# Optimization experiments

Measured on AMD Instinct MI355X. Metric: run time of the kernel, lower is better.

## Reference

```python
import jax, jax.numpy as jnp
import numpy as np

T, B, E, H = 2048, 4, 1024, 16
HD = E // H
SCALE = HD ** -0.5


def setup_inputs() -> dict:
    key = jax.random.key(0)
    k1, k2, k3 = jax.random.split(key, 3)
    # xavier-ish scaling on weights for numerical sanity
    inputs = jax.random.normal(k1, (T, B, E), dtype=jnp.float32)
    in_proj_weight = jax.random.normal(k2, (3 * E, E), dtype=jnp.float32) * (2.0 / (4 * E)) ** 0.5
    out_proj_weight = jax.random.normal(k3, (E, E), dtype=jnp.float32) * (1.0 / E) ** 0.5
    return {"inputs": inputs, "in_proj_weight": in_proj_weight, "out_proj_weight": out_proj_weight}


def reference(inputs, in_proj_weight, out_proj_weight):
    t, b, e = inputs.shape
    # fused QKV projection: [T,B,E] @ [E,3E] -> [T, B*H, 3, HD]
    qkv = jnp.einsum('tbe,fe->tbf', inputs, in_proj_weight)
    qkv = qkv.reshape(t, b * H, 3, HD)
    q, k, v = qkv[:, :, 0, :], qkv[:, :, 1, :], qkv[:, :, 2, :]  # [T, B*H, HD]
    # scaled attention scores per (batch*head): [B*H, T, T]
    scores = SCALE * jnp.einsum('tnd,snd->nts', q, k)
    probs = jax.nn.softmax(scores, axis=-1)
    # dropout p=0.0 -> identity
    ctx = jnp.einsum('nts,snd->tnd', probs, v).reshape(t, b, e)
    # output projection (applied to attention context, matching intended math / backward)
    return jnp.einsum('tbe,oe->tbo', ctx, out_proj_weight)
```

## Files before the change

kernel.cpp:

```cpp
#include <hip/hip_runtime.h>
#include <stdint.h>
#include <stddef.h>


typedef __attribute__((ext_vector_type(8))) short bf16x8;
typedef __attribute__((ext_vector_type(4))) float f32x4;
typedef __attribute__((ext_vector_type(4))) unsigned int u32x4;

#define MFMA16(a, b, c) __builtin_amdgcn_mfma_f32_16x16x32_bf16((a), (b), (c), 0, 0, 0)

__device__ __forceinline__ unsigned short f2bf(float f) {
  unsigned u = __builtin_bit_cast(unsigned, f);
  u += 0x7fffu + ((u >> 16) & 1u);
  return (unsigned short)(u >> 16);
}

__device__ __forceinline__ float fast_exp2(float x) {
#if __has_builtin(__builtin_amdgcn_exp2f)
  return __builtin_amdgcn_exp2f(x);
#else
  return exp2f(x);
#endif
}

__device__ __forceinline__ unsigned cvtpk(float lo, float hi) {
  unsigned r;
  asm volatile("v_cvt_pk_bf16_f32 %0, %1, %2" : "=v"(r) : "v"(lo), "v"(hi));
  return r;
}

__device__ __forceinline__ void lane_swap32(unsigned &a, unsigned &b) {
#if __has_builtin(__builtin_amdgcn_permlane32_swap)
  auto r = __builtin_amdgcn_permlane32_swap(a, b, false, false);
  a = r[0]; b = r[1];
#else
  const bool hi = (threadIdx.x & 32) != 0;
  unsigned sa = (unsigned)__shfl_xor((int)a, 32, 64);
  unsigned sb = (unsigned)__shfl_xor((int)b, 32, 64);
  unsigned na = hi ? sb : a;
  unsigned nb = hi ? b : sa;
  a = na; b = nb;
#endif
}

__device__ __forceinline__ void lane_swap16(unsigned &a, unsigned &b) {
#if __has_builtin(__builtin_amdgcn_permlane16_swap)
  auto r = __builtin_amdgcn_permlane16_swap(a, b, false, false);
  a = r[0]; b = r[1];
#else
  const bool odd = (threadIdx.x & 16) != 0;
  unsigned sa = (unsigned)__shfl_xor((int)a, 16, 64);
  unsigned sb = (unsigned)__shfl_xor((int)b, 16, 64);
  unsigned na = odd ? sb : a;
  unsigned nb = odd ? b : sa;
  a = na; b = nb;
#endif
}

__device__ __forceinline__ void gload_lds16(const void* g, void* l) {
  __builtin_amdgcn_global_load_lds((const __attribute__((address_space(1))) void*)g,
                                   (__attribute__((address_space(3))) void*)l,
                                   16, 0, 0);
}

__global__ __launch_bounds__(256) void k_cvt(const float* __restrict__ src,
                                             unsigned short* __restrict__ dst, int n4) {
  int i = blockIdx.x * 256 + threadIdx.x;
  if (i >= n4) return;
  const float4 v = ((const float4*)src)[i];
  ushort4 o;
  o.x = f2bf(v.x); o.y = f2bf(v.y); o.z = f2bf(v.z); o.w = f2bf(v.w);
  ((ushort4*)dst)[i] = o;
}

__global__ __launch_bounds__(256, 2) void k_gemm_qkv(
    const unsigned short* __restrict__ A,
    const unsigned short* __restrict__ Bt,
    unsigned short* __restrict__ Qb,
    unsigned short* __restrict__ Kb,
    unsigned short* __restrict__ Vb) {
  constexpr int K = 1024;
  __shared__ __align__(16) unsigned short As[128 * 32];
  __shared__ __align__(16) unsigned short Bs[128 * 32];
  const int tid = threadIdx.x;
  const int l = tid & 63, w = tid >> 6;
  const int lr = l & 15, lg = l >> 4;
  const int bm = blockIdx.x, bn = blockIdx.y;
  const int wr = (w >> 1) * 64, wc = (w & 1) * 64;

  f32x4 acc[4][4] = {};

  const int o0 = tid * 16, o1 = tid * 16 + 4096;
  const int r0 = o0 >> 6, c0 = o0 & 63;
  const int r1 = o1 >> 6, c1 = o1 & 63;
  const char* gA0 = (const char*)A + (size_t)(bm * 128 + r0) * (K * 2) + c0;
  const char* gA1 = (const char*)A + (size_t)(bm * 128 + r1) * (K * 2) + c1;
  const char* gB0 = (const char*)Bt + (size_t)(bn * 128 + r0) * (K * 2) + c0;
  const char* gB1 = (const char*)Bt + (size_t)(bn * 128 + r1) * (K * 2) + c1;
  char* lA0 = (char*)As + o0;
  char* lA1 = (char*)As + o1;
  char* lB0 = (char*)Bs + o0;
  char* lB1 = (char*)Bs + o1;

  for (int kt = 0; kt < K / 32; ++kt) {
    const int kb = kt * 64;
    gload_lds16(gA0 + kb, lA0);
    gload_lds16(gA1 + kb, lA1);
    gload_lds16(gB0 + kb, lB0);
    gload_lds16(gB1 + kb, lB1);
    __syncthreads();
    bf16x8 af[4], bfr[4];
#pragma unroll
    for (int mf = 0; mf < 4; ++mf)
      af[mf] = *(const bf16x8*)&As[(wr + mf * 16 + lr) * 32 + lg * 8];
#pragma unroll
    for (int nf = 0; nf < 4; ++nf)
      bfr[nf] = *(const bf16x8*)&Bs[(wc + nf * 16 + lr) * 32 + lg * 8];
#pragma unroll
    for (int mf = 0; mf < 4; ++mf)
#pragma unroll
      for (int nf = 0; nf < 4; ++nf)
        acc[mf][nf] = MFMA16(af[mf], bfr[nf], acc[mf][nf]);
    __syncthreads();
  }

#pragma unroll
  for (int nf = 0; nf < 4; ++nf) {
    const int f = bn * 128 + wc + nf * 16 + lr;
    const int hq = f / 192;
    const int s3 = (f >> 6) % 3;
    const int d = f & 63;
    unsigned short* dst = (s3 == 0) ? Qb : (s3 == 1) ? Kb : Vb;
    const float qscale = (s3 == 0) ? 0.18033688011112042f : 1.0f;
#pragma unroll
    for (int mf = 0; mf < 4; ++mf) {
#pragma unroll
      for (int i = 0; i < 4; ++i) {
        const int r = bm * 128 + wr + mf * 16 + lg * 4 + i;
        const int t = r >> 2, bb2 = r & 3;
        const int nIdx = bb2 * 16 + hq;
        dst[((size_t)nIdx * 2048 + t) * 64 + d] = f2bf(acc[mf][nf][i] * qscale);
      }
    }
  }
}

__global__ __launch_bounds__(256) void k_vtrans(const unsigned short* __restrict__ V,
                                                unsigned short* __restrict__ VT) {
  __shared__ unsigned short tile[64][66];
  const int tid = threadIdx.x;
  const int n = blockIdx.y, t0 = blockIdx.x * 64;
  const int r = tid >> 2, c0 = (tid & 3) * 16;
  const unsigned short* src = V + ((size_t)(n * 2048 + t0 + r) * 64 + c0);
  bf16x8 a = *(const bf16x8*)src;
  bf16x8 b = *(const bf16x8*)(src + 8);
#pragma unroll
  for (int j = 0; j < 8; ++j) tile[r][c0 + j] = (unsigned short)a[j];
#pragma unroll
  for (int j = 0; j < 8; ++j) tile[r][c0 + 8 + j] = (unsigned short)b[j];
  __syncthreads();
  const int d = tid >> 2, u0 = (tid & 3) * 16;
  bf16x8 oA, oB;
#pragma unroll
  for (int j = 0; j < 8; ++j) oA[j] = (short)tile[u0 + j][d];
#pragma unroll
  for (int j = 0; j < 8; ++j) oB[j] = (short)tile[u0 + 8 + j][d];
  unsigned short* dst = VT + ((size_t)(n * 64 + d) * 2048 + t0 + u0);
  *(bf16x8*)dst = oA;
  *(bf16x8*)(dst + 8) = oB;
}

__global__ __launch_bounds__(256, 2) void k_attn(
    const unsigned short* __restrict__ Qb, const unsigned short* __restrict__ Kb,
    const unsigned short* __restrict__ VTb, unsigned short* __restrict__ Cx) {
  __shared__ __align__(16) unsigned short Ks[2][64 * 64];
  __shared__ __align__(16) unsigned short Vt[2][64 * 64];

  const int tid = threadIdx.x;
  const int l = tid & 63, w = tid >> 6;
  const int lq = l & 15, lg = l >> 4;
  const int n = blockIdx.x, qt = blockIdx.y;

  const unsigned short* Qh = Qb + (size_t)n * (2048 * 64);
  const unsigned short* Kh = Kb + (size_t)n * (2048 * 64);
  const unsigned short* Vh = VTb + (size_t)n * (64 * 2048);

  bf16x8 aq[4][2];
#pragma unroll
  for (int qf = 0; qf < 4; ++qf)
#pragma unroll
    for (int kd = 0; kd < 2; ++kd)
      aq[qf][kd] = *(const bf16x8*)&Qh[(size_t)(qt * 256 + w * 64 + qf * 16 + lq) * 64 +
                                       kd * 32 + lg * 8];

  f32x4 o[4][4] = {};
  float lsum[4] = {0.f, 0.f, 0.f, 0.f};

  char* Ksl = (char*)&Ks[0][0];
  char* Vtl = (char*)&Vt[0][0];

  auto STAGE = [&](int buf, int st) {
    const int s0 = st * 64;
#pragma unroll
    for (int it = 0; it < 2; ++it) {
      const int off = (it * 256 + tid) * 16;
      const int row = off >> 7;
      const int colb = (off & 127) ^ ((row & 7) << 4);
      gload_lds16((const char*)Kh + ((size_t)(s0 + row) << 7) + colb, Ksl + buf * 8192 + off);
      gload_lds16((const char*)Vh + ((size_t)row << 12) + (s0 << 1) + colb, Vtl + buf * 8192 + off);
    }
  };

  STAGE(0, 0);
  asm volatile("s_waitcnt vmcnt(0)" ::: "memory");
  __builtin_amdgcn_s_barrier();

#pragma unroll 2
  for (int st = 0; st < 32; ++st) {
    const int cur = st & 1;
    if (st + 1 < 32) STAGE(cur ^ 1, st + 1);

    const char* Kc = Ksl + cur * 8192;
    const char* Vc = Vtl + cur * 8192;

    __builtin_amdgcn_s_setprio(1);
#pragma unroll
    for (int kb = 0; kb < 2; ++kb) {
      bf16x8 kf[2][2];
#pragma unroll
      for (int sfl = 0; sfl < 2; ++sfl) {
        const int rowk = (2 * kb + sfl) * 16 + lq;
        const int sw = (rowk & 7) << 4;
        kf[sfl][0] = *(const bf16x8*)(Kc + ((rowk * 128 + lg * 16) ^ sw));
        kf[sfl][1] = *(const bf16x8*)(Kc + ((rowk * 128 + 64 + lg * 16) ^ sw));
      }

      bf16x8 pq[4];
#pragma unroll
      for (int qf = 0; qf < 4; ++qf) {
        f32x4 s0 = {0.f, 0.f, 0.f, 0.f};
        f32x4 s1 = {0.f, 0.f, 0.f, 0.f};
        s0 = MFMA16(kf[0][0], aq[qf][0], s0);
        s0 = MFMA16(kf[0][1], aq[qf][1], s0);
        s1 = MFMA16(kf[1][0], aq[qf][0], s1);
        s1 = MFMA16(kf[1][1], aq[qf][1], s1);
        float accs = 0.f;
#pragma unroll
        for (int i = 0; i < 4; ++i) {
          s0[i] = fast_exp2(s0[i]);
          s1[i] = fast_exp2(s1[i]);
          accs += s0[i] + s1[i];
        }
        lsum[qf] += accs;
        unsigned w0 = cvtpk(s0[0], s0[1]);
        unsigned w1 = cvtpk(s0[2], s0[3]);
        unsigned w2 = cvtpk(s1[0], s1[1]);
        unsigned w3 = cvtpk(s1[2], s1[3]);
        lane_swap32(w0, w2);
        lane_swap32(w1, w3);
        lane_swap16(w0, w2);
        lane_swap16(w1, w3);
        u32x4 t4 = {w0, w1, w2, w3};
        pq[qf] = __builtin_bit_cast(bf16x8, t4);
      }

#pragma unroll
      for (int df = 0; df < 4; ++df) {
        const int rowd = df * 16 + lq;
        const int sw = (rowd & 7) << 4;
        bf16x8 vf = *(const bf16x8*)(Vc + ((rowd * 128 + kb * 64 + lg * 16) ^ sw));
#pragma unroll
        for (int qf = 0; qf < 4; ++qf)
          o[df][qf] = MFMA16(vf, pq[qf], o[df][qf]);
      }
    }
    __builtin_amdgcn_s_setprio(0);

    asm volatile("s_waitcnt vmcnt(0)" ::: "memory");
    __builtin_amdgcn_s_barrier();
  }

  const int bb = n >> 4, h = n & 15;
#pragma unroll
  for (int qf = 0; qf < 4; ++qf) {
    float li = lsum[qf];
    li += __shfl_xor(li, 16, 64);
    li += __shfl_xor(li, 32, 64);
    const float inv = 1.0f / li;
    const int q = qt * 256 + w * 64 + qf * 16 + lq;
#pragma unroll
    for (int df = 0; df < 4; ++df) {
      ushort4 pk;
      pk.x = f2bf(o[df][qf][0] * inv);
      pk.y = f2bf(o[df][qf][1] * inv);
      pk.z = f2bf(o[df][qf][2] * inv);
      pk.w = f2bf(o[df][qf][3] * inv);
      *(ushort4*)&Cx[(size_t)(q * 4 + bb) * 1024 + h * 64 + df * 16 + lg * 4] = pk;
    }
  }
}

__global__ __launch_bounds__(256, 2) void k_gemm_out(
    const unsigned short* __restrict__ A,
    const unsigned short* __restrict__ Bt,
    float* __restrict__ C) {
  constexpr int K = 1024;
  __shared__ __align__(16) unsigned short As[128 * 32];
  __shared__ __align__(16) unsigned short Bs[128 * 32];
  const int tid = threadIdx.x;
  const int l = tid & 63, w = tid >> 6;
  const int lr = l & 15, lg = l >> 4;
  const int bm = blockIdx.x, bn = blockIdx.y;
  const int wr = (w >> 1) * 64, wc = (w & 1) * 64;

  f32x4 acc[4][4] = {};

  const int o0 = tid * 16, o1 = tid * 16 + 4096;
  const int r0 = o0 >> 6, c0 = o0 & 63;
  const int r1 = o1 >> 6, c1 = o1 & 63;
  const char* gA0 = (const char*)A + (size_t)(bm * 128 + r0) * (K * 2) + c0;
  const char* gA1 = (const char*)A + (size_t)(bm * 128 + r1) * (K * 2) + c1;
  const char* gB0 = (const char*)Bt + (size_t)(bn * 128 + r0) * (K * 2) + c0;
  const char* gB1 = (const char*)Bt + (size_t)(bn * 128 + r1) * (K * 2) + c1;
  char* lA0 = (char*)As + o0;
  char* lA1 = (char*)As + o1;
  char* lB0 = (char*)Bs + o0;
  char* lB1 = (char*)Bs + o1;

  for (int kt = 0; kt < K / 32; ++kt) {
    const int kb = kt * 64;
    gload_lds16(gA0 + kb, lA0);
    gload_lds16(gA1 + kb, lA1);
    gload_lds16(gB0 + kb, lB0);
    gload_lds16(gB1 + kb, lB1);
    __syncthreads();
    bf16x8 af[4], bfr[4];
#pragma unroll
    for (int mf = 0; mf < 4; ++mf)
      af[mf] = *(const bf16x8*)&As[(wr + mf * 16 + lr) * 32 + lg * 8];
#pragma unroll
    for (int nf = 0; nf < 4; ++nf)
      bfr[nf] = *(const bf16x8*)&Bs[(wc + nf * 16 + lr) * 32 + lg * 8];
#pragma unroll
    for (int mf = 0; mf < 4; ++mf)
#pragma unroll
      for (int nf = 0; nf < 4; ++nf)
        acc[mf][nf] = MFMA16(af[mf], bfr[nf], acc[mf][nf]);
    __syncthreads();
  }

#pragma unroll
  for (int mf = 0; mf < 4; ++mf)
#pragma unroll
    for (int i = 0; i < 4; ++i) {
      const int r = bm * 128 + wr + mf * 16 + lg * 4 + i;
#pragma unroll
      for (int nf = 0; nf < 4; ++nf)
        C[(size_t)r * 1024 + bn * 128 + wc + nf * 16 + lr] = acc[mf][nf][i];
    }
}

extern "C" void kernel_launch(void* const* d_in, const int* in_sizes, int n_in,
                              void* d_out, int out_size, void* d_ws, size_t ws_size,
                              hipStream_t stream) {
  const float* X = (const float*)d_in[0];
  const float* W1 = (const float*)d_in[1];
  const float* Wo = (const float*)d_in[2];
  float* out = (float*)d_out;

  char* ws = (char*)d_ws;
  unsigned short* Xb  = (unsigned short*)(ws);
  unsigned short* W1b = (unsigned short*)(ws + 16777216);
  unsigned short* Wob = (unsigned short*)(ws + 23068672);
  unsigned short* Qb  = (unsigned short*)(ws + 25165824);
  unsigned short* Kb  = (unsigned short*)(ws + 41943040);
  unsigned short* VTb = (unsigned short*)(ws + 58720256);
  unsigned short* Vb  = (unsigned short*)(ws + 75497472);
  unsigned short* Cx  = (unsigned short*)(ws + 75497472);

  k_cvt<<<8192, 256, 0, stream>>>(X, Xb, 2097152);
  k_cvt<<<3072, 256, 0, stream>>>(W1, W1b, 786432);
  k_cvt<<<1024, 256, 0, stream>>>(Wo, Wob, 262144);
  k_gemm_qkv<<<dim3(64, 24), 256, 0, stream>>>(Xb, W1b, Qb, Kb, Vb);
  k_vtrans<<<dim3(32, 64), 256, 0, stream>>>(Vb, VTb);
  k_attn<<<dim3(64, 8), 256, 0, stream>>>(Qb, Kb, VTb, Cx);
  k_gemm_out<<<dim3(64, 8), 256, 0, stream>>>(Cx, Wob, out);
}
```

Before: 197.9 us.

## Fuse V transpose into QKV GEMM epilogue and merge conversion kernels

The QKV GEMM epilogue now stages V tiles in shared memory and writes V directly in transposed layout, so the separate V-transpose kernel and its global round trip go away. The three fp32-to-bf16 conversion launches are merged into a single kernel, cutting launch overhead. The cost is a larger shared-memory footprint in the GEMM, an extra barrier, and a per-block branch on the Q/K/V segment. The transposed stores are 8-byte ushort4 writes, which are less coalesced than the old 16-byte writes.

New measurement: 186.7 us. -5.6%, faster.

```diff
diff --git a/kernel.cpp b/kernel.cpp
--- a/kernel.cpp
+++ b/kernel.cpp
@@ -63,14 +63,23 @@
                                    16, 0, 0);
 }
 
-__global__ __launch_bounds__(256) void k_cvt(const float* __restrict__ src,
-                                             unsigned short* __restrict__ dst, int n4) {
+__global__ __launch_bounds__(256) void k_cvt3(const float* __restrict__ X,
+                                              const float* __restrict__ W1,
+                                              const float* __restrict__ Wo,
+                                              unsigned short* __restrict__ Xb,
+                                              unsigned short* __restrict__ W1b,
+                                              unsigned short* __restrict__ Wob) {
   int i = blockIdx.x * 256 + threadIdx.x;
-  if (i >= n4) return;
-  const float4 v = ((const float4*)src)[i];
+  const float* src;
+  unsigned short* dst;
+  int j;
+  if (i < 2097152) { src = X; dst = Xb; j = i; }
+  else if (i < 2097152 + 786432) { src = W1; dst = W1b; j = i - 2097152; }
+  else { src = Wo; dst = Wob; j = i - (2097152 + 786432); }
+  const float4 v = ((const float4*)src)[j];
   ushort4 o;
   o.x = f2bf(v.x); o.y = f2bf(v.y); o.z = f2bf(v.z); o.w = f2bf(v.w);
-  ((ushort4*)dst)[i] = o;
+  ((ushort4*)dst)[j] = o;
 }
 
 __global__ __launch_bounds__(256, 2) void k_gemm_qkv(
@@ -78,10 +87,12 @@
     const unsigned short* __restrict__ Bt,
     unsigned short* __restrict__ Qb,
     unsigned short* __restrict__ Kb,
-    unsigned short* __restrict__ Vb) {
+    unsigned short* __restrict__ VTb) {
   constexpr int K = 1024;
-  __shared__ __align__(16) unsigned short As[128 * 32];
-  __shared__ __align__(16) unsigned short Bs[128 * 32];
+  __shared__ __align__(16) unsigned short Sm[8704];
+  unsigned short* As = Sm;
+  unsigned short* Bs = Sm + 4096;
+
   const int tid = threadIdx.x;
   const int l = tid & 63, w = tid >> 6;
   const int lr = l & 15, lg = l >> 4;
@@ -124,50 +135,58 @@
     __syncthreads();
   }
 
-#pragma unroll
-  for (int nf = 0; nf < 4; ++nf) {
-    const int f = bn * 128 + wc + nf * 16 + lr;
-    const int hq = f / 192;
-    const int s3 = (f >> 6) % 3;
-    const int d = f & 63;
-    unsigned short* dst = (s3 == 0) ? Qb : (s3 == 1) ? Kb : Vb;
-    const float qscale = (s3 == 0) ? 0.18033688011112042f : 1.0f;
-#pragma unroll
-    for (int mf = 0; mf < 4; ++mf) {
-#pragma unroll
-      for (int i = 0; i < 4; ++i) {
-        const int r = bm * 128 + wr + mf * 16 + lg * 4 + i;
-        const int t = r >> 2, bb2 = r & 3;
-        const int nIdx = bb2 * 16 + hq;
-        dst[((size_t)nIdx * 2048 + t) * 64 + d] = f2bf(acc[mf][nf][i] * qscale);
-      }
-    }
-  }
-}
-
-__global__ __launch_bounds__(256) void k_vtrans(const unsigned short* __restrict__ V,
-                                                unsigned short* __restrict__ VT) {
-  __shared__ unsigned short tile[64][66];
-  const int tid = threadIdx.x;
-  const int n = blockIdx.y, t0 = blockIdx.x * 64;
-  const int r = tid >> 2, c0 = (tid & 3) * 16;
-  const unsigned short* src = V + ((size_t)(n * 2048 + t0 + r) * 64 + c0);
-  bf16x8 a = *(const bf16x8*)src;
-  bf16x8 b = *(const bf16x8*)(src + 8);
-#pragma unroll
-  for (int j = 0; j < 8; ++j) tile[r][c0 + j] = (unsigned short)a[j];
-#pragma unroll
-  for (int j = 0; j < 8; ++j) tile[r][c0 + 8 + j] = (unsigned short)b[j];
+  const int f0 = bn * 128 + wc;
+  const int s3g = (f0 >> 6) % 3;
+  const int hqg = f0 / 192;
+
+  if (s3g != 2) {
+    unsigned short* dst = (s3g == 0) ? Qb : Kb;
+    const float qscale = (s3g == 0) ? 0.18033688011112042f : 1.0f;
+#pragma unroll
+    for (int nf = 0; nf < 4; ++nf) {
+      const int d = nf * 16 + lr;
+#pragma unroll
+      for (int mf = 0; mf < 4; ++mf) {
+#pragma unroll
+        for (int i = 0; i < 4; ++i) {
+          const int r = bm * 128 + wr + mf * 16 + lg * 4 + i;
+          const int t = r >> 2, bb2 = r & 3;
+          dst[((size_t)(bb2 * 16 + hqg) * 2048 + t) * 64 + d] = f2bf(acc[mf][nf][i] * qscale);
+        }
+      }
+    }
+  } else {
+#pragma unroll
+    for (int nf = 0; nf < 4; ++nf) {
+      const int d = nf * 16 + lr;
+#pragma unroll
+      for (int mf = 0; mf < 4; ++mf) {
+#pragma unroll
+        for (int i = 0; i < 4; ++i) {
+          const int rl = wr + mf * 16 + lg * 4 + i;
+          Sm[rl * 68 + d] = f2bf(acc[mf][nf][i]);
+        }
+      }
+    }
+  }
   __syncthreads();
-  const int d = tid >> 2, u0 = (tid & 3) * 16;
-  bf16x8 oA, oB;
-#pragma unroll
-  for (int j = 0; j < 8; ++j) oA[j] = (short)tile[u0 + j][d];
-#pragma unroll
-  for (int j = 0; j < 8; ++j) oB[j] = (short)tile[u0 + 8 + j][d];
-  unsigned short* dst = VT + ((size_t)(n * 64 + d) * 2048 + t0 + u0);
-  *(bf16x8*)dst = oA;
-  *(bf16x8*)(dst + 8) = oB;
+  if (s3g == 2) {
+    const int u = (w >> 1) * 64 + l;
+    const int d = u >> 1, th = u & 1;
+#pragma unroll
+    for (int bb = 0; bb < 4; ++bb) {
+      const size_t base = ((size_t)(bb * 16 + hqg) * 64 + d) * 2048 + bm * 32 + th * 16;
+#pragma unroll
+      for (int tq = 0; tq < 4; ++tq) {
+        ushort4 pk;
+        pk.x = Sm[((th * 16 + tq * 4 + 0) * 4 + bb) * 68 + d];
+        pk.y = Sm[((th * 16 + tq * 4 + 1) * 4 + bb) * 68 + d];
+        pk.z = Sm[((th * 16 + tq * 4 + 2) * 4 + bb) * 68 + d];
+        pk.w = Sm[((th * 16 + tq * 4 + 3) * 4 + bb) * 68 + d];
+        *(ushort4*)&VTb[base + tq * 4] = pk;
+      }
+    }
+  }
 }
 
 __global__ __launch_bounds__(256, 2) void k_attn(
@@ -375,14 +394,10 @@
   unsigned short* Qb  = (unsigned short*)(ws + 25165824);
   unsigned short* Kb  = (unsigned short*)(ws + 41943040);
   unsigned short* VTb = (unsigned short*)(ws + 58720256);
-  unsigned short* Vb  = (unsigned short*)(ws + 75497472);
   unsigned short* Cx  = (unsigned short*)(ws + 75497472);
 
-  k_cvt<<<8192, 256, 0, stream>>>(X, Xb, 2097152);
-  k_cvt<<<3072, 256, 0, stream>>>(W1, W1b, 786432);
-  k_cvt<<<1024, 256, 0, stream>>>(Wo, Wob, 262144);
-  k_gemm_qkv<<<dim3(64, 24), 256, 0, stream>>>(Xb, W1b, Qb, Kb, Vb);
-  k_vtrans<<<dim3(32, 64), 256, 0, stream>>>(Vb, VTb);
+  k_cvt3<<<12288, 256, 0, stream>>>(X, W1, Wo, Xb, W1b, Wob);
+  k_gemm_qkv<<<dim3(64, 24), 256, 0, stream>>>(Xb, W1b, Qb, Kb, VTb);
   k_attn<<<dim3(64, 8), 256, 0, stream>>>(Qb, Kb, VTb, Cx);
   k_gemm_out<<<dim3(64, 8), 256, 0, stream>>>(Cx, Wob, out);
 }
```
